# Performance work log

Hardware: AMD Instinct MI355X
Metric: run time of the kernel (lower is better)

Reference implementation:

```python
import jax, jax.numpy as jnp
import numpy as np

N_NODES = 100000
NEG_SLOPE = 0.2
EPS = 1e-16


def gat_conv(x, src, dst, W, a_src, a_dst, bias, heads, out_dim, concat):
    # x: [N, F]; src/dst: [Etot] (self loops already appended)
    N = x.shape[0]
    h = (x @ W).reshape(N, heads, out_dim)          # [N, H, D]
    alpha_src = jnp.einsum('nhd,hd->nh', h, a_src)  # [N, H]
    alpha_dst = jnp.einsum('nhd,hd->nh', h, a_dst)  # [N, H]
    e = alpha_src[src] + alpha_dst[dst]             # [E, H]
    e = jnp.where(e > 0, e, NEG_SLOPE * e)          # leaky_relu
    # segment softmax over incoming edges of each dst node
    m = jax.ops.segment_max(e, dst, num_segments=N)
    e = jnp.exp(e - m[dst])
    s = jax.ops.segment_sum(e, dst, num_segments=N)
    alpha = e / (s[dst] + EPS)                      # [E, H]
    msg = h[src] * alpha[:, :, None]                # [E, H, D]
    out = jax.ops.segment_sum(msg, dst, num_segments=N)  # [N, H, D]
    if concat:
        out = out.reshape(N, heads * out_dim)
    else:
        out = out.mean(axis=1)
    return out + bias


def setup_inputs() -> dict:
    key = jax.random.key(0)
    ks = jax.random.split(key, 10)
    F_in, H1, D1 = 256, 8, 8
    D2 = 256 // 2  # hidden_features // 2
    x = jax.random.normal(ks[0], (N_NODES, F_in), dtype=jnp.float32)
    edge_index = jax.random.randint(ks[1], (2, 1600000), 0, N_NODES, dtype=jnp.int64)
    sc1 = 1.0 / np.sqrt(F_in)
    sc2 = 1.0 / np.sqrt(H1 * D1)
    return {
        'x': x,
        'edge_index': edge_index,
        'W1': jax.random.normal(ks[2], (F_in, H1 * D1), dtype=jnp.float32) * sc1,
        'a_src1': jax.random.normal(ks[3], (H1, D1), dtype=jnp.float32) * 0.1,
        'a_dst1': jax.random.normal(ks[4], (H1, D1), dtype=jnp.float32) * 0.1,
        'b1': jnp.zeros((H1 * D1,), dtype=jnp.float32),
        'W2': jax.random.normal(ks[5], (H1 * D1, D2), dtype=jnp.float32) * sc2,
        'a_src2': jax.random.normal(ks[6], (1, D2), dtype=jnp.float32) * 0.1,
        'a_dst2': jax.random.normal(ks[7], (1, D2), dtype=jnp.float32) * 0.1,
        'b2': jnp.zeros((D2,), dtype=jnp.float32),
    }


def reference(x, edge_index, W1, a_src1, a_dst1, b1, W2, a_src2, a_dst2, b2):
    # GAT.encode in eval mode (dropout p=0.6 disabled)
    N = x.shape[0]
    loop = jnp.arange(N, dtype=edge_index.dtype)
    src = jnp.concatenate([edge_index[0], loop])  # PyG add_self_loops
    dst = jnp.concatenate([edge_index[1], loop])
    h = gat_conv(x, src, dst, W1, a_src1, a_dst1, b1, heads=8, out_dim=8, concat=True)
    h = jax.nn.elu(h)
    z = gat_conv(h, src, dst, W2, a_src2, a_dst2, b2, heads=1, out_dim=128, concat=False)
    return z
```

## Files before the change

### kernel.cpp

```cpp
#include <hip/hip_runtime.h>
#include <hip/hip_bf16.h>
#include <cstdint>

#define H1 8
#define C1 64
#define D2 128
#define FIN 256
#define NEG 0.2f
#define EPSS 1e-16f
#define CH 1024
#define NPW2 8
#define NPB2 32
#define XPAD 264
#define HP 68
#define NPBIN 128
#define TILEB 4096
#define MAXD1 128
#define MAXD2 256

template<typename T> __device__ __forceinline__ float toF(T v);
template<> __device__ __forceinline__ float toF<float>(float v) { return v; }
template<> __device__ __forceinline__ float toF<__hip_bfloat16>(__hip_bfloat16 v) { return __bfloat162float(v); }
template<typename T> __device__ __forceinline__ T fromF(float v);
template<> __device__ __forceinline__ float fromF<float>(float v) { return v; }
template<> __device__ __forceinline__ __hip_bfloat16 fromF<__hip_bfloat16>(float v) { return __float2bfloat16(v); }

__device__ __forceinline__ float bcast_lane(float v, int lane) {
    return __int_as_float(__builtin_amdgcn_readlane(__float_as_int(v), lane));
}

__device__ __forceinline__ unsigned pk_bf16(float lo, float hi) {
    unsigned a = (unsigned)__bfloat16_as_ushort(__float2bfloat16(lo));
    unsigned b = (unsigned)__bfloat16_as_ushort(__float2bfloat16(hi));
    return a | (b << 16);
}

typedef __attribute__((ext_vector_type(8))) short bf16x8;
typedef __attribute__((ext_vector_type(4))) float f32x4;

__device__ __forceinline__ void chain_upd(float ev, float hv,
                                          float& m, float& s, float& a)
{
    float mn = fmaxf(m, ev);
    float sc = __expf(m - mn);
    float p  = __expf(ev - mn);
    s = fmaf(s, sc, p);
    a = fmaf(a, sc, p * hv);
    m = mn;
}

template<typename T>
__global__ __launch_bounds__(256) void k_gemm1(const float* __restrict__ x,
    const float* __restrict__ W1, const float* __restrict__ a_src1,
    const float* __restrict__ a_dst1, T* __restrict__ h1,
    float* __restrict__ asrc1, float* __restrict__ adst1, int N)
{
    __shared__ alignas(16) unsigned short Xs[64 * XPAD];
    __shared__ alignas(16) unsigned short Wt[64 * XPAD];
    int tid = threadIdx.x;
    int wave = tid >> 6, lane = tid & 63;
    int nodeBase = blockIdx.x * 64;

    {
        int c = tid & 63;
        int kb = (tid >> 6) * 4;
        #pragma unroll
        for (int s = 0; s < 16; ++s) {
            int k0 = s * 16 + kb;
            float f0 = W1[(k0 + 0) * C1 + c];
            float f1 = W1[(k0 + 1) * C1 + c];
            float f2 = W1[(k0 + 2) * C1 + c];
            float f3 = W1[(k0 + 3) * C1 + c];
            *reinterpret_cast<uint2*>(&Wt[c * XPAD + k0]) =
                make_uint2(pk_bf16(f0, f1), pk_bf16(f2, f3));
        }
    }
    for (int i = tid; i < 64 * 64; i += 256) {
        int r = i >> 6, kq = i & 63;
        int n = nodeBase + r;
        float4 v = (n < N) ? reinterpret_cast<const float4*>(x)[(size_t)n * 64 + kq]
                           : make_float4(0.f, 0.f, 0.f, 0.f);
        *reinterpret_cast<uint2*>(&Xs[r * XPAD + kq * 4]) =
            make_uint2(pk_bf16(v.x, v.y), pk_bf16(v.z, v.w));
    }
    __syncthreads();

    int m = lane & 15;
    int kg = lane >> 4;
    int arow = wave * 16 + m;
    f32x4 acc[4];
    #pragma unroll
    for (int t = 0; t < 4; ++t) acc[t] = (f32x4){0.f, 0.f, 0.f, 0.f};
    #pragma unroll
    for (int ks = 0; ks < 8; ++ks) {
        int k0 = ks * 32 + kg * 8;
        bf16x8 a = *reinterpret_cast<const bf16x8*>(&Xs[arow * XPAD + k0]);
        #pragma unroll
        for (int t = 0; t < 4; ++t) {
            bf16x8 b = *reinterpret_cast<const bf16x8*>(&Wt[(t * 16 + m) * XPAD + k0]);
            acc[t] = __builtin_amdgcn_mfma_f32_16x16x32_bf16(a, b, acc[t], 0, 0, 0);
        }
    }
    __syncthreads();

    float* Hs = reinterpret_cast<float*>(Xs);
    int crow = (lane >> 4) * 4;
    #pragma unroll
    for (int t = 0; t < 4; ++t)
        #pragma unroll
        for (int r = 0; r < 4; ++r)
            Hs[(wave * 16 + crow + r) * HP + t * 16 + m] = acc[t][r];
    __syncthreads();

    float as_l = a_src1[lane], ad_l = a_dst1[lane];
    int n0 = nodeBase + wave * 16;
    #pragma unroll
    for (int i = 0; i < 16; ++i) {
        int n = n0 + i;
        if (n >= N) break;
        float hv = Hs[(wave * 16 + i) * HP + lane];
        h1[(size_t)n * C1 + lane] = fromF<T>(hv);
        float vs = hv * as_l, vd = hv * ad_l;
        #pragma unroll
        for (int off = 1; off < 8; off <<= 1) {
            vs += __shfl_xor(vs, off);
            vd += __shfl_xor(vd, off);
        }
        if ((lane & 7) == 0) {
            asrc1[n * H1 + (lane >> 3)] = vs;
            adst1[n * H1 + (lane >> 3)] = vd;
        }
    }
}

__global__ __launch_bounds__(128) void k_wvec(const float* __restrict__ W2,
    const float* __restrict__ a_src2, const float* __restrict__ a_dst2,
    float* __restrict__ wsrc, float* __restrict__ wdst)
{
    int t = threadIdx.x;
    int k = t & 63;
    const float* a = (t < 64) ? a_src2 : a_dst2;
    float s = 0.f;
    for (int c = 0; c < D2; ++c) s = fmaf(W2[k * D2 + c], a[c], s);
    if (t < 64) wsrc[k] = s; else wdst[k] = s;
}

__global__ __launch_bounds__(256) void k_binhist(const int* __restrict__ ei, int E, int N,
    int nbins, int* __restrict__ binCnt)
{
    __shared__ int lcnt[1024];
    int tot = E + N;
    int t0 = blockIdx.x * TILEB;
    int cnt = min(TILEB, tot - t0);
    for (int i = threadIdx.x; i < nbins; i += 256) lcnt[i] = 0;
    __syncthreads();
    for (int i = threadIdx.x; i < cnt; i += 256) {
        int e = t0 + i;
        int dst = (e < E) ? ei[(size_t)E + e] : (e - E);
        atomicAdd(&lcnt[dst >> 7], 1);
    }
    __syncthreads();
    for (int i = threadIdx.x; i < nbins; i += 256)
        if (lcnt[i]) atomicAdd(&binCnt[i], lcnt[i]);
}

__global__ __launch_bounds__(256) void k_binscan(const int* __restrict__ binCnt,
    int* __restrict__ binOff, int* __restrict__ binCur, int nbins)
{
    __shared__ int wtot[4];
    int t = threadIdx.x, lane = t & 63, wave = t >> 6;
    int v[4];
    #pragma unroll
    for (int j = 0; j < 4; ++j) {
        int idx = t * 4 + j;
        v[j] = (idx < nbins) ? binCnt[idx] : 0;
    }
    int s = v[0] + v[1] + v[2] + v[3];
    int incl = s;
    #pragma unroll
    for (int off = 1; off < 64; off <<= 1) {
        int tt = __shfl_up(incl, off);
        if (lane >= off) incl += tt;
    }
    if (lane == 63) wtot[wave] = incl;
    __syncthreads();
    int woff = 0;
    #pragma unroll
    for (int w = 0; w < 4; ++w) if (w < wave) woff += wtot[w];
    int run = woff + incl - s;
    #pragma unroll
    for (int j = 0; j < 4; ++j) {
        int idx = t * 4 + j;
        if (idx < nbins) { binOff[idx] = run; binCur[idx] = run; }
        run += v[j];
    }
    if (t == 255) binOff[nbins] = woff + incl;
}

__global__ __launch_bounds__(256) void k_bin(const int* __restrict__ ei, int E, int N,
    int nbins, int* __restrict__ binCur, int* __restrict__ binned)
{
    __shared__ int recs[TILEB];
    __shared__ unsigned short bns[TILEB];
    __shared__ int lcnt[1024];
    __shared__ int lbase[1024];
    int tot = E + N;
    int t0 = blockIdx.x * TILEB;
    int cnt = min(TILEB, tot - t0);
    for (int i = threadIdx.x; i < nbins; i += 256) lcnt[i] = 0;
    __syncthreads();
    for (int i = threadIdx.x; i < cnt; i += 256) {
        int e = t0 + i;
        int src, dst;
        if (e < E) { src = ei[e]; dst = ei[(size_t)E + e]; }
        else       { src = e - E; dst = src; }
        int b = dst >> 7;
        recs[i] = src | ((dst & 127) << 17);
        bns[i] = (unsigned short)b;
        atomicAdd(&lcnt[b], 1);
    }
    __syncthreads();
    for (int i = threadIdx.x; i < nbins; i += 256) {
        int c = lcnt[i];
        if (c) lbase[i] = atomicAdd(&binCur[i], c);
        lcnt[i] = 0;
    }
    __syncthreads();
    for (int i = threadIdx.x; i < cnt; i += 256) {
        int b = bns[i];
        int lp = atomicAdd(&lcnt[b], 1);
        binned[lbase[b] + lp] = recs[i];
    }
}

__global__ __launch_bounds__(256) void k_bindeg(const int* __restrict__ binOff,
    const int* __restrict__ binned, int* __restrict__ deg, int N)
{
    __shared__ int cnt[NPBIN];
    int b = blockIdx.x;
    int s0 = binOff[b], s1 = binOff[b + 1];
    if (threadIdx.x < NPBIN) cnt[threadIdx.x] = 0;
    __syncthreads();
    for (int i = s0 + threadIdx.x; i < s1; i += 256)
        atomicAdd(&cnt[binned[i] >> 17], 1);
    __syncthreads();
    int node = b * NPBIN + threadIdx.x;
    if (threadIdx.x < NPBIN && node < N) deg[node] = cnt[threadIdx.x];
}

__global__ __launch_bounds__(256) void k_binscatter(const int* __restrict__ binOff,
    const int* __restrict__ binned, const int* __restrict__ ptr,
    int* __restrict__ edge_src, int N)
{
    __shared__ int cur[NPBIN];
    int b = blockIdx.x;
    int base = b * NPBIN;
    if (threadIdx.x < NPBIN) {
        int node = base + threadIdx.x;
        cur[threadIdx.x] = (node < N) ? ptr[node] : 0;
    }
    __syncthreads();
    int s0 = binOff[b], s1 = binOff[b + 1];
    for (int i = s0 + threadIdx.x; i < s1; i += 256) {
        int rec = binned[i];
        int p = atomicAdd(&cur[rec >> 17], 1);
        edge_src[p] = rec & 0x1FFFF;
    }
}

__global__ void k_count(const int* __restrict__ ei, int E, int N,
                        int* __restrict__ deg)
{
    int tot = E + N;
    for (int e = blockIdx.x * blockDim.x + threadIdx.x; e < tot;
         e += gridDim.x * blockDim.x) {
        int dst = (e < E) ? ei[(size_t)E + e] : (e - E);
        atomicAdd(&deg[dst], 1);
    }
}

__global__ void k_scatter(const int* __restrict__ ei, int E, int N,
                          int* __restrict__ cursor, int* __restrict__ edge_src)
{
    int tot = E + N;
    for (int e = blockIdx.x * blockDim.x + threadIdx.x; e < tot;
         e += gridDim.x * blockDim.x) {
        int src, dst;
        if (e < E) { src = ei[e]; dst = ei[(size_t)E + e]; }
        else       { src = e - E; dst = e - E; }
        int pos = atomicAdd(&cursor[dst], 1);
        edge_src[pos] = src;
    }
}

__global__ __launch_bounds__(256) void k_scanA(const int* __restrict__ deg,
    int* __restrict__ ptr, int* __restrict__ chunkSum)
{
    __shared__ int wtot[4];
    int b = blockIdx.x, t = threadIdx.x;
    int lane = t & 63, wave = t >> 6;
    int4 v = reinterpret_cast<const int4*>(deg + (size_t)b * CH)[t];
    int s = v.x + v.y + v.z + v.w;
    int incl = s;
    #pragma unroll
    for (int off = 1; off < 64; off <<= 1) {
        int tt = __shfl_up(incl, off);
        if (lane >= off) incl += tt;
    }
    if (lane == 63) wtot[wave] = incl;
    __syncthreads();
    int woff = 0;
    #pragma unroll
    for (int w = 0; w < 4; ++w) if (w < wave) woff += wtot[w];
    int excl = woff + incl - s;
    int i0 = b * CH + t * 4;
    ptr[i0 + 0] = excl;
    ptr[i0 + 1] = excl + v.x;
    ptr[i0 + 2] = excl + v.x + v.y;
    ptr[i0 + 3] = excl + v.x + v.y + v.z;
    if (t == 255) chunkSum[b] = woff + incl;
}

__global__ void k_scanB(const int* __restrict__ chunkSum, int* __restrict__ chunkOff,
                        int NB, int* __restrict__ ptrN)
{
    if (threadIdx.x == 0) {
        int c = 0;
        for (int b = 0; b < NB; ++b) { chunkOff[b] = c; c += chunkSum[b]; }
        *ptrN = c;
    }
}

__global__ __launch_bounds__(256) void k_scanC(int* __restrict__ ptr,
    int* __restrict__ cursor, const int* __restrict__ chunkOff, int N)
{
    int b = blockIdx.x;
    int off = chunkOff[b];
    int i0 = b * CH + threadIdx.x * 4;
    #pragma unroll
    for (int k = 0; k < 4; ++k) {
        int i = i0 + k;
        if (i < N) { int v = ptr[i] + off; ptr[i] = v; cursor[i] = v; }
    }
}

template<typename T>
__global__ __launch_bounds__(256) void k_agg1(const int* __restrict__ ptr,
    const int* __restrict__ edge_src, const T* __restrict__ h1,
    const float* __restrict__ asrc1, const float* __restrict__ adst1,
    const float* __restrict__ b1, const float* __restrict__ wsrc,
    const float* __restrict__ wdst, T* __restrict__ hmid,
    float* __restrict__ asrc2, float* __restrict__ adst2, int N)
{
    __shared__ float S1[4 * MAXD1 * H1];
    int wave = threadIdx.x >> 6, lane = threadIdx.x & 63;
    float* st = S1 + wave * (MAXD1 * H1);
    int n = blockIdx.x * 4 + wave;
    if (n >= N) return;
    int start = ptr[n], end = ptr[n + 1];
    int deg = end - start;
    int h = lane >> 3;
    float o;

    if (deg <= MAXD1) {
        int e_loc = lane >> 3, hh = lane & 7;
        float adsth = adst1[n * H1 + hh];
        float mloc = -1e30f;
        for (int eb = start, base = 0; eb < end; eb += 8, base += 64) {
            int e = eb + e_loc;
            float ev = -1e30f;
            if (e < end) {
                int s = edge_src[e];
                ev = asrc1[s * H1 + hh] + adsth;
                ev = ev > 0.f ? ev : NEG * ev;
                st[base + lane] = ev;
            }
            mloc = fmaxf(mloc, ev);
        }
        mloc = fmaxf(mloc, __shfl_xor(mloc, 8));
        mloc = fmaxf(mloc, __shfl_xor(mloc, 16));
        mloc = fmaxf(mloc, __shfl_xor(mloc, 32));
        __builtin_amdgcn_wave_barrier();
        float sloc = 0.f;
        for (int eb = start, base = 0; eb < end; eb += 8, base += 64) {
            if (eb + e_loc < end) {
                float p = __expf(st[base + lane] - mloc);
                st[base + lane] = p;
                sloc += p;
            }
        }
        sloc += __shfl_xor(sloc, 8);
        sloc += __shfl_xor(sloc, 16);
        sloc += __shfl_xor(sloc, 32);
        float inv = 1.f / (sloc + EPSS);
        __builtin_amdgcn_wave_barrier();
        float inv_c = __shfl(inv, h);

        float a0 = 0.f, a1 = 0.f, a2 = 0.f, a3 = 0.f;
        float a4 = 0.f, a5 = 0.f, a6 = 0.f, a7 = 0.f;
        int e = start;
        for (; e + 8 <= end; e += 8) {
            int r = e - start;
            int i0 = edge_src[e + 0]; int i1 = edge_src[e + 1];
            int i2 = edge_src[e + 2]; int i3 = edge_src[e + 3];
            int i4 = edge_src[e + 4]; int i5 = edge_src[e + 5];
            int i6 = edge_src[e + 6]; int i7 = edge_src[e + 7];
            float w0 = st[(r + 0) * H1 + h]; float w1 = st[(r + 1) * H1 + h];
            float w2 = st[(r + 2) * H1 + h]; float w3 = st[(r + 3) * H1 + h];
            float w4 = st[(r + 4) * H1 + h]; float w5 = st[(r + 5) * H1 + h];
            float w6 = st[(r + 6) * H1 + h]; float w7 = st[(r + 7) * H1 + h];
            a0 = fmaf(w0, toF(h1[((size_t)(unsigned)i0 << 6) + lane]), a0);
            a1 = fmaf(w1, toF(h1[((size_t)(unsigned)i1 << 6) + lane]), a1);
            a2 = fmaf(w2, toF(h1[((size_t)(unsigned)i2 << 6) + lane]), a2);
            a3 = fmaf(w3, toF(h1[((size_t)(unsigned)i3 << 6) + lane]), a3);
            a4 = fmaf(w4, toF(h1[((size_t)(unsigned)i4 << 6) + lane]), a4);
            a5 = fmaf(w5, toF(h1[((size_t)(unsigned)i5 << 6) + lane]), a5);
            a6 = fmaf(w6, toF(h1[((size_t)(unsigned)i6 << 6) + lane]), a6);
            a7 = fmaf(w7, toF(h1[((size_t)(unsigned)i7 << 6) + lane]), a7);
        }
        for (; e < end; ++e) {
            int s = edge_src[e];
            a0 = fmaf(st[(e - start) * H1 + h],
                      toF(h1[((size_t)(unsigned)s << 6) + lane]), a0);
        }
        float acc = ((a0 + a1) + (a2 + a3)) + ((a4 + a5) + (a6 + a7));
        o = acc * inv_c;
    } else {
        float adst = adst1[n * H1 + h];
        float m[8], ss[8], aa[8];
        #pragma unroll
        for (int j = 0; j < 8; ++j) { m[j] = -1e30f; ss[j] = 0.f; aa[j] = 0.f; }
        int e = start;
        for (; e + 8 <= end; e += 8) {
            int idx[8];
            #pragma unroll
            for (int j = 0; j < 8; ++j) idx[j] = edge_src[e + j];
            #pragma unroll
            for (int j = 0; j < 8; ++j) {
                float t = asrc1[idx[j] * H1 + h] + adst;
                t = t > 0.f ? t : NEG * t;
                chain_upd(t, toF(h1[((size_t)(unsigned)idx[j] << 6) + lane]),
                          m[j], ss[j], aa[j]);
            }
        }
        for (; e < end; ++e) {
            int s = edge_src[e];
            float t = asrc1[s * H1 + h] + adst;
            t = t > 0.f ? t : NEG * t;
            chain_upd(t, toF(h1[((size_t)(unsigned)s << 6) + lane]), m[0], ss[0], aa[0]);
        }
        float M = fmaxf(fmaxf(fmaxf(m[0], m[1]), fmaxf(m[2], m[3])),
                        fmaxf(fmaxf(m[4], m[5]), fmaxf(m[6], m[7])));
        float sum = 0.f, acc = 0.f;
        #pragma unroll
        for (int j = 0; j < 8; ++j) {
            float sc = __expf(m[j] - M);
            sum = fmaf(ss[j], sc, sum);
            acc = fmaf(aa[j], sc, acc);
        }
        o = acc / (sum + EPSS);
    }

    o = o + b1[lane];
    o = o > 0.f ? o : (expf(o) - 1.f);
    hmid[(size_t)n * C1 + lane] = fromF<T>(o);
    float vs = o * wsrc[lane];
    float vd = o * wdst[lane];
    #pragma unroll
    for (int off = 1; off < 64; off <<= 1) {
        vs += __shfl_xor(vs, off);
        vd += __shfl_xor(vd, off);
    }
    if (lane == 0) { asrc2[n] = vs; adst2[n] = vd; }
}

template<typename T>
__global__ __launch_bounds__(256) void k_agg2(const int* __restrict__ ptr,
    const int* __restrict__ edge_src, const T* __restrict__ hmid,
    const float* __restrict__ asrc2, const float* __restrict__ adst2,
    T* __restrict__ aggv_out, int N)
{
    __shared__ float S2[4 * MAXD2];
    int wave = threadIdx.x >> 6, lane = threadIdx.x & 63;
    float* st = S2 + wave * MAXD2;
    int n = blockIdx.x * 4 + wave;
    if (n >= N) return;
    int start = ptr[n], end = ptr[n + 1];
    int deg = end - start;
    float adst = adst2[n];
    float aggv;

    if (deg <= MAXD2) {
        float mloc = -1e30f;
        for (int e = start + lane; e < end; e += 64) {
            int s = edge_src[e];
            float ev = asrc2[s] + adst;
            ev = ev > 0.f ? ev : NEG * ev;
            st[e - start] = ev;
            mloc = fmaxf(mloc, ev);
        }
        #pragma unroll
        for (int off = 1; off < 64; off <<= 1)
            mloc = fmaxf(mloc, __shfl_xor(mloc, off));
        __builtin_amdgcn_wave_barrier();
        float sloc = 0.f;
        for (int e = start + lane; e < end; e += 64) {
            float p = __expf(st[e - start] - mloc);
            st[e - start] = p;
            sloc += p;
        }
        #pragma unroll
        for (int off = 1; off < 64; off <<= 1)
            sloc += __shfl_xor(sloc, off);
        float inv = 1.f / (sloc + EPSS);
        __builtin_amdgcn_wave_barrier();

        float a0 = 0.f, a1 = 0.f, a2 = 0.f, a3 = 0.f;
        float a4 = 0.f, a5 = 0.f, a6 = 0.f, a7 = 0.f;
        int e = start;
        for (; e + 8 <= end; e += 8) {
            int r = e - start;
            int i0 = edge_src[e + 0]; int i1 = edge_src[e + 1];
            int i2 = edge_src[e + 2]; int i3 = edge_src[e + 3];
            int i4 = edge_src[e + 4]; int i5 = edge_src[e + 5];
            int i6 = edge_src[e + 6]; int i7 = edge_src[e + 7];
            a0 = fmaf(st[r + 0], toF(hmid[((size_t)(unsigned)i0 << 6) + lane]), a0);
            a1 = fmaf(st[r + 1], toF(hmid[((size_t)(unsigned)i1 << 6) + lane]), a1);
            a2 = fmaf(st[r + 2], toF(hmid[((size_t)(unsigned)i2 << 6) + lane]), a2);
            a3 = fmaf(st[r + 3], toF(hmid[((size_t)(unsigned)i3 << 6) + lane]), a3);
            a4 = fmaf(st[r + 4], toF(hmid[((size_t)(unsigned)i4 << 6) + lane]), a4);
            a5 = fmaf(st[r + 5], toF(hmid[((size_t)(unsigned)i5 << 6) + lane]), a5);
            a6 = fmaf(st[r + 6], toF(hmid[((size_t)(unsigned)i6 << 6) + lane]), a6);
            a7 = fmaf(st[r + 7], toF(hmid[((size_t)(unsigned)i7 << 6) + lane]), a7);
        }
        for (; e < end; ++e) {
            int s = edge_src[e];
            a0 = fmaf(st[e - start], toF(hmid[((size_t)(unsigned)s << 6) + lane]), a0);
        }
        float acc = ((a0 + a1) + (a2 + a3)) + ((a4 + a5) + (a6 + a7));
        aggv = acc * inv;
    } else {
        float m[8], ss[8], aa[8];
        #pragma unroll
        for (int j = 0; j < 8; ++j) { m[j] = -1e30f; ss[j] = 0.f; aa[j] = 0.f; }
        int e = start;
        for (; e + 8 <= end; e += 8) {
            int idx[8];
            #pragma unroll
            for (int j = 0; j < 8; ++j) idx[j] = edge_src[e + j];
            #pragma unroll
            for (int j = 0; j < 8; ++j) {
                float t = asrc2[idx[j]] + adst;
                t = t > 0.f ? t : NEG * t;
                chain_upd(t, toF(hmid[((size_t)(unsigned)idx[j] << 6) + lane]),
                          m[j], ss[j], aa[j]);
            }
        }
        for (; e < end; ++e) {
            int s = edge_src[e];
            float t = asrc2[s] + adst;
            t = t > 0.f ? t : NEG * t;
            chain_upd(t, toF(hmid[((size_t)(unsigned)s << 6) + lane]), m[0], ss[0], aa[0]);
        }
        float M = fmaxf(fmaxf(fmaxf(m[0], m[1]), fmaxf(m[2], m[3])),
                        fmaxf(fmaxf(m[4], m[5]), fmaxf(m[6], m[7])));
        float sum = 0.f, acc = 0.f;
        #pragma unroll
        for (int j = 0; j < 8; ++j) {
            float sc = __expf(m[j] - M);
            sum = fmaf(ss[j], sc, sum);
            acc = fmaf(aa[j], sc, acc);
        }
        aggv = acc / (sum + EPSS);
    }
    aggv_out[(size_t)n * C1 + lane] = fromF<T>(aggv);
}

template<typename T>
__global__ __launch_bounds__(256) void k_gemm2(const T* __restrict__ aggv,
    const float* __restrict__ W2, const float* __restrict__ b2,
    float* __restrict__ out, int N)
{
    __shared__ float Ws[C1 * D2];
    for (int i = threadIdx.x; i < C1 * D2 / 4; i += 256)
        reinterpret_cast<float4*>(Ws)[i] = reinterpret_cast<const float4*>(W2)[i];

    int wave = threadIdx.x >> 6, lane = threadIdx.x & 63;
    int n0 = blockIdx.x * NPB2 + wave * NPW2;

    float av[NPW2];
    #pragma unroll
    for (int j = 0; j < NPW2; ++j) {
        int n = n0 + j;
        av[j] = (n < N) ? toF(aggv[(size_t)n * C1 + lane]) : 0.f;
    }
    __syncthreads();

    float acc0[NPW2], acc1[NPW2];
    #pragma unroll
    for (int j = 0; j < NPW2; ++j) { acc0[j] = 0.f; acc1[j] = 0.f; }

    #pragma unroll 4
    for (int k = 0; k < 64; ++k) {
        float w0 = Ws[k * D2 + lane];
        float w1 = Ws[k * D2 + 64 + lane];
        #pragma unroll
        for (int j = 0; j < NPW2; ++j) {
            float xk = bcast_lane(av[j], k);
            acc0[j] = fmaf(xk, w0, acc0[j]);
            acc1[j] = fmaf(xk, w1, acc1[j]);
        }
    }

    float bb0 = b2[lane], bb1 = b2[64 + lane];
    #pragma unroll
    for (int j = 0; j < NPW2; ++j) {
        int n = n0 + j;
        if (n >= N) continue;
        out[(size_t)n * D2 + lane]      = acc0[j] + bb0;
        out[(size_t)n * D2 + 64 + lane] = acc1[j] + bb1;
    }
}

extern "C" void kernel_launch(void* const* d_in, const int* in_sizes, int n_in,
                              void* d_out, int out_size, void* d_ws, size_t ws_size,
                              hipStream_t stream)
{
    const float* x      = (const float*)d_in[0];
    const int*   ei     = (const int*)d_in[1];
    const float* W1     = (const float*)d_in[2];
    const float* a_src1 = (const float*)d_in[3];
    const float* a_dst1 = (const float*)d_in[4];
    const float* b1     = (const float*)d_in[5];
    const float* W2     = (const float*)d_in[6];
    const float* a_src2 = (const float*)d_in[7];
    const float* a_dst2 = (const float*)d_in[8];
    const float* b2     = (const float*)d_in[9];
    float* out = (float*)d_out;

    const int N = in_sizes[0] / FIN;
    const int E = in_sizes[1] / 2;
    const int Etot = E + N;
    const int NB = (N + CH - 1) / CH;
    const size_t NP = (size_t)NB * CH;

    const size_t common =
        ((size_t)N * H1 * 4 + 255 & ~(size_t)255) * 2 +
        (((size_t)N * 4 + 255) & ~(size_t)255) * 2 +
        512 +
        (((size_t)NP * 4 + 255) & ~(size_t)255) * 2 +
        (((size_t)(NP + 1) * 4 + 255) & ~(size_t)255) +
        (((size_t)NB * 4 + 255) & ~(size_t)255) * 2 +
        (((size_t)Etot * 4 + 255) & ~(size_t)255) +
        4096;
    const bool f32path = ws_size >= common + 2 * ((size_t)N * C1 * 4 + 256);

    char* ws = (char*)d_ws;
    size_t off = 0;
    auto alloc = [&](size_t bytes) -> void* {
        void* p = ws + off;
        off = (off + bytes + 255) & ~(size_t)255;
        return p;
    };
    const size_t es = f32path ? 4 : 2;
    void*  h1v    = alloc((size_t)N * C1 * es);
    void*  hmidv  = alloc((size_t)N * C1 * es);
    float* asrc1  = (float*)alloc((size_t)N * H1 * 4);
    float* adst1  = (float*)alloc((size_t)N * H1 * 4);
    float* asrc2  = (float*)alloc((size_t)N * 4);
    float* adst2  = (float*)alloc((size_t)N * 4);
    float* wsrc   = (float*)alloc(64 * 4);
    float* wdst   = (float*)alloc(64 * 4);
    int*   deg    = (int*)alloc(NP * 4);
    int*   ptr    = (int*)alloc((NP + 1) * 4);
    int*   cursor = (int*)alloc(NP * 4);
    int*   chunkSum = (int*)alloc((size_t)NB * 4);
    int*   chunkOff = (int*)alloc((size_t)NB * 4);
    int*   edge_src = (int*)alloc((size_t)Etot * 4);

    const int nodeBlocks = (N + 3) / 4;
    const int g1Blocks = (N + 63) / 64;
    const int g2Blocks = (N + NPB2 - 1) / NPB2;

    const int nbins = (N + NPBIN - 1) / NPBIN;
    const bool binpath = (N <= (1 << 17)) &&
                         ((size_t)Etot * 4 <= (size_t)N * C1 * es);
    hipMemsetAsync(deg, 0, NP * 4, stream);
    if (binpath) {
        int* binned = (int*)h1v;
        int* binCnt = (int*)hmidv;
        int* binOff = binCnt + 1056;
        int* binCur = binOff + 1056;
        const int binBlocks = (Etot + TILEB - 1) / TILEB;
        hipMemsetAsync(binCnt, 0, (size_t)nbins * 4, stream);
        k_binhist<<<binBlocks, 256, 0, stream>>>(ei, E, N, nbins, binCnt);
        k_binscan<<<1, 256, 0, stream>>>(binCnt, binOff, binCur, nbins);
        k_bin<<<binBlocks, 256, 0, stream>>>(ei, E, N, nbins, binCur, binned);
        k_bindeg<<<nbins, 256, 0, stream>>>(binOff, binned, deg, N);
        k_scanA<<<NB, 256, 0, stream>>>(deg, ptr, chunkSum);
        k_scanB<<<1, 64, 0, stream>>>(chunkSum, chunkOff, NB, ptr + N);
        k_scanC<<<NB, 256, 0, stream>>>(ptr, cursor, chunkOff, N);
        k_binscatter<<<nbins, 256, 0, stream>>>(binOff, binned, ptr, edge_src, N);
    } else {
        k_count<<<2048, 256, 0, stream>>>(ei, E, N, deg);
        k_scanA<<<NB, 256, 0, stream>>>(deg, ptr, chunkSum);
        k_scanB<<<1, 64, 0, stream>>>(chunkSum, chunkOff, NB, ptr + N);
        k_scanC<<<NB, 256, 0, stream>>>(ptr, cursor, chunkOff, N);
        k_scatter<<<2048, 256, 0, stream>>>(ei, E, N, cursor, edge_src);
    }

    k_wvec<<<1, 128, 0, stream>>>(W2, a_src2, a_dst2, wsrc, wdst);

    if (f32path) {
        float* h1 = (float*)h1v; float* hmid = (float*)hmidv;
        k_gemm1<float><<<g1Blocks, 256, 0, stream>>>(x, W1, a_src1, a_dst1, h1, asrc1, adst1, N);
        k_agg1<float><<<nodeBlocks, 256, 0, stream>>>(ptr, edge_src, h1, asrc1, adst1, b1,
                                                      wsrc, wdst, hmid, asrc2, adst2, N);
        float* aggv = (float*)h1v;
        k_agg2<float><<<nodeBlocks, 256, 0, stream>>>(ptr, edge_src, hmid, asrc2, adst2, aggv, N);
        k_gemm2<float><<<g2Blocks, 256, 0, stream>>>(aggv, W2, b2, out, N);
    } else {
        __hip_bfloat16* h1 = (__hip_bfloat16*)h1v; __hip_bfloat16* hmid = (__hip_bfloat16*)hmidv;
        k_gemm1<__hip_bfloat16><<<g1Blocks, 256, 0, stream>>>(x, W1, a_src1, a_dst1, h1, asrc1, adst1, N);
        k_agg1<__hip_bfloat16><<<nodeBlocks, 256, 0, stream>>>(ptr, edge_src, h1, asrc1, adst1, b1,
                                                               wsrc, wdst, hmid, asrc2, adst2, N);
        __hip_bfloat16* aggv = (__hip_bfloat16*)h1v;
        k_agg2<__hip_bfloat16><<<nodeBlocks, 256, 0, stream>>>(ptr, edge_src, hmid, asrc2, adst2, aggv, N);
        k_gemm2<__hip_bfloat16><<<g2Blocks, 256, 0, stream>>>(aggv, W2, b2, out, N);
    }
}
```

Baseline: 371.2 us.

## Fuse bin degree count, CSR scan and scatter into one kernel; deepen gather unroll

The binned CSR build now runs as a single kernel per bin. It counts per-node degrees in shared memory, does a local wave prefix scan offset by the bin's global start, writes ptr and scatters edge sources. This replaces the degree kernel, the three-kernel global scan and the separate scatter kernel, along with the memset of deg, which cuts launches and global round trips. Separately, the aggregation loops in both layers gain a 16-edge unrolled stage that issues all gathers before the FMAs to raise memory-level parallelism, at some cost in register pressure.

Result: faster. 358.9 us (-3.3%).

```diff
diff --git a/kernel.cpp b/kernel.cpp
--- a/kernel.cpp
+++ b/kernel.cpp
@@ -233,35 +233,43 @@
     }
 }
 
-__global__ __launch_bounds__(256) void k_bindeg(const int* __restrict__ binOff,
-    const int* __restrict__ binned, int* __restrict__ deg, int N)
+__global__ __launch_bounds__(256) void k_binptr(const int* __restrict__ binOff,
+    const int* __restrict__ binned, int* __restrict__ ptr,
+    int* __restrict__ edge_src, int N, int nbins)
 {
     __shared__ int cnt[NPBIN];
-    int b = blockIdx.x;
+    __shared__ int cur[NPBIN];
+    __shared__ int w0tot;
+    int b = blockIdx.x, t = threadIdx.x;
     int s0 = binOff[b], s1 = binOff[b + 1];
-    if (threadIdx.x < NPBIN) cnt[threadIdx.x] = 0;
-    __syncthreads();
-    for (int i = s0 + threadIdx.x; i < s1; i += 256)
+    if (t < NPBIN) cnt[t] = 0;
+    __syncthreads();
+    for (int i = s0 + t; i < s1; i += 256)
         atomicAdd(&cnt[binned[i] >> 17], 1);
     __syncthreads();
-    int node = b * NPBIN + threadIdx.x;
-    if (threadIdx.x < NPBIN && node < N) deg[node] = cnt[threadIdx.x];
-}
-
-__global__ __launch_bounds__(256) void k_binscatter(const int* __restrict__ binOff,
-    const int* __restrict__ binned, const int* __restrict__ ptr,
-    int* __restrict__ edge_src, int N)
-{
-    __shared__ int cur[NPBIN];
-    int b = blockIdx.x;
-    int base = b * NPBIN;
-    if (threadIdx.x < NPBIN) {
-        int node = base + threadIdx.x;
-        cur[threadIdx.x] = (node < N) ? ptr[node] : 0;
-    }
-    __syncthreads();
-    int s0 = binOff[b], s1 = binOff[b + 1];
-    for (int i = s0 + threadIdx.x; i < s1; i += 256) {
+    int v = 0, incl = 0;
+    if (t < NPBIN) {
+        int lane = t & 63;
+        v = cnt[t];
+        incl = v;
+        #pragma unroll
+        for (int off = 1; off < 64; off <<= 1) {
+            int tt = __shfl_up(incl, off);
+            if (lane >= off) incl += tt;
+        }
+        if (t == 63) w0tot = incl;
+    }
+    __syncthreads();
+    if (t < NPBIN) {
+        int base = s0 + ((t >= 64) ? w0tot : 0);
+        int excl = base + incl - v;
+        int node = b * NPBIN + t;
+        if (node < N) ptr[node] = excl;
+        cur[t] = excl;
+    }
+    if (b == nbins - 1 && t == 0) ptr[N] = s1;
+    __syncthreads();
+    for (int i = s0 + t; i < s1; i += 256) {
         int rec = binned[i];
         int p = atomicAdd(&cur[rec >> 17], 1);
         edge_src[p] = rec & 0x1FFFF;
@@ -399,24 +407,44 @@
         float a0 = 0.f, a1 = 0.f, a2 = 0.f, a3 = 0.f;
         float a4 = 0.f, a5 = 0.f, a6 = 0.f, a7 = 0.f;
         int e = start;
+        for (; e + 16 <= end; e += 16) {
+            int r = e - start;
+            int idx[16];
+            #pragma unroll
+            for (int j = 0; j < 16; ++j) idx[j] = edge_src[e + j];
+            float hv[16];
+            #pragma unroll
+            for (int j = 0; j < 16; ++j)
+                hv[j] = toF(h1[((size_t)(unsigned)idx[j] << 6) + lane]);
+            float w[16];
+            #pragma unroll
+            for (int j = 0; j < 16; ++j) w[j] = st[(r + j) * H1 + h];
+            a0 = fmaf(w[0],  hv[0],  a0); a1 = fmaf(w[1],  hv[1],  a1);
+            a2 = fmaf(w[2],  hv[2],  a2); a3 = fmaf(w[3],  hv[3],  a3);
+            a4 = fmaf(w[4],  hv[4],  a4); a5 = fmaf(w[5],  hv[5],  a5);
+            a6 = fmaf(w[6],  hv[6],  a6); a7 = fmaf(w[7],  hv[7],  a7);
+            a0 = fmaf(w[8],  hv[8],  a0); a1 = fmaf(w[9],  hv[9],  a1);
+            a2 = fmaf(w[10], hv[10], a2); a3 = fmaf(w[11], hv[11], a3);
+            a4 = fmaf(w[12], hv[12], a4); a5 = fmaf(w[13], hv[13], a5);
+            a6 = fmaf(w[14], hv[14], a6); a7 = fmaf(w[15], hv[15], a7);
+        }
         for (; e + 8 <= end; e += 8) {
             int r = e - start;
-            int i0 = edge_src[e + 0]; int i1 = edge_src[e + 1];
-            int i2 = edge_src[e + 2]; int i3 = edge_src[e + 3];
-            int i4 = edge_src[e + 4]; int i5 = edge_src[e + 5];
-            int i6 = edge_src[e + 6]; int i7 = edge_src[e + 7];
-            float w0 = st[(r + 0) * H1 + h]; float w1 = st[(r + 1) * H1 + h];
-            float w2 = st[(r + 2) * H1 + h]; float w3 = st[(r + 3) * H1 + h];
-            float w4 = st[(r + 4) * H1 + h]; float w5 = st[(r + 5) * H1 + h];
-            float w6 = st[(r + 6) * H1 + h]; float w7 = st[(r + 7) * H1 + h];
-            a0 = fmaf(w0, toF(h1[((size_t)(unsigned)i0 << 6) + lane]), a0);
-            a1 = fmaf(w1, toF(h1[((size_t)(unsigned)i1 << 6) + lane]), a1);
-            a2 = fmaf(w2, toF(h1[((size_t)(unsigned)i2 << 6) + lane]), a2);
-            a3 = fmaf(w3, toF(h1[((size_t)(unsigned)i3 << 6) + lane]), a3);
-            a4 = fmaf(w4, toF(h1[((size_t)(unsigned)i4 << 6) + lane]), a4);
-            a5 = fmaf(w5, toF(h1[((size_t)(unsigned)i5 << 6) + lane]), a5);
-            a6 = fmaf(w6, toF(h1[((size_t)(unsigned)i6 << 6) + lane]), a6);
-            a7 = fmaf(w7, toF(h1[((size_t)(unsigned)i7 << 6) + lane]), a7);
+            int idx[8];
+            #pragma unroll
+            for (int j = 0; j < 8; ++j) idx[j] = edge_src[e + j];
+            float hv[8];
+            #pragma unroll
+            for (int j = 0; j < 8; ++j)
+                hv[j] = toF(h1[((size_t)(unsigned)idx[j] << 6) + lane]);
+            a0 = fmaf(st[(r + 0) * H1 + h], hv[0], a0);
+            a1 = fmaf(st[(r + 1) * H1 + h], hv[1], a1);
+            a2 = fmaf(st[(r + 2) * H1 + h], hv[2], a2);
+            a3 = fmaf(st[(r + 3) * H1 + h], hv[3], a3);
+            a4 = fmaf(st[(r + 4) * H1 + h], hv[4], a4);
+            a5 = fmaf(st[(r + 5) * H1 + h], hv[5], a5);
+            a6 = fmaf(st[(r + 6) * H1 + h], hv[6], a6);
+            a7 = fmaf(st[(r + 7) * H1 + h], hv[7], a7);
         }
         for (; e < end; ++e) {
             int s = edge_src[e];
@@ -518,20 +546,37 @@
         float a0 = 0.f, a1 = 0.f, a2 = 0.f, a3 = 0.f;
         float a4 = 0.f, a5 = 0.f, a6 = 0.f, a7 = 0.f;
         int e = start;
+        for (; e + 16 <= end; e += 16) {
+            int r = e - start;
+            int idx[16];
+            #pragma unroll
+            for (int j = 0; j < 16; ++j) idx[j] = edge_src[e + j];
+            float hv[16];
+            #pragma unroll
+            for (int j = 0; j < 16; ++j)
+                hv[j] = toF(hmid[((size_t)(unsigned)idx[j] << 6) + lane]);
+            a0 = fmaf(st[r + 0],  hv[0],  a0); a1 = fmaf(st[r + 1],  hv[1],  a1);
+            a2 = fmaf(st[r + 2],  hv[2],  a2); a3 = fmaf(st[r + 3],  hv[3],  a3);
+            a4 = fmaf(st[r + 4],  hv[4],  a4); a5 = fmaf(st[r + 5],  hv[5],  a5);
+            a6 = fmaf(st[r + 6],  hv[6],  a6); a7 = fmaf(st[r + 7],  hv[7],  a7);
+            a0 = fmaf(st[r + 8],  hv[8],  a0); a1 = fmaf(st[r + 9],  hv[9],  a1);
+            a2 = fmaf(st[r + 10], hv[10], a2); a3 = fmaf(st[r + 11], hv[11], a3);
+            a4 = fmaf(st[r + 12], hv[12], a4); a5 = fmaf(st[r + 13], hv[13], a5);
+            a6 = fmaf(st[r + 14], hv[14], a6); a7 = fmaf(st[r + 15], hv[15], a7);
+        }
         for (; e + 8 <= end; e += 8) {
             int r = e - start;
-            int i0 = edge_src[e + 0]; int i1 = edge_src[e + 1];
-            int i2 = edge_src[e + 2]; int i3 = edge_src[e + 3];
-            int i4 = edge_src[e + 4]; int i5 = edge_src[e + 5];
-            int i6 = edge_src[e + 6]; int i7 = edge_src[e + 7];
-            a0 = fmaf(st[r + 0], toF(hmid[((size_t)(unsigned)i0 << 6) + lane]), a0);
-            a1 = fmaf(st[r + 1], toF(hmid[((size_t)(unsigned)i1 << 6) + lane]), a1);
-            a2 = fmaf(st[r + 2], toF(hmid[((size_t)(unsigned)i2 << 6) + lane]), a2);
-            a3 = fmaf(st[r + 3], toF(hmid[((size_t)(unsigned)i3 << 6) + lane]), a3);
-            a4 = fmaf(st[r + 4], toF(hmid[((size_t)(unsigned)i4 << 6) + lane]), a4);
-            a5 = fmaf(st[r + 5], toF(hmid[((size_t)(unsigned)i5 << 6) + lane]), a5);
-            a6 = fmaf(st[r + 6], toF(hmid[((size_t)(unsigned)i6 << 6) + lane]), a6);
-            a7 = fmaf(st[r + 7], toF(hmid[((size_t)(unsigned)i7 << 6) + lane]), a7);
+            int idx[8];
+            #pragma unroll
+            for (int j = 0; j < 8; ++j) idx[j] = edge_src[e + j];
+            float hv[8];
+            #pragma unroll
+            for (int j = 0; j < 8; ++j)
+                hv[j] = toF(hmid[((size_t)(unsigned)idx[j] << 6) + lane]);
+            a0 = fmaf(st[r + 0], hv[0], a0); a1 = fmaf(st[r + 1], hv[1], a1);
+            a2 = fmaf(st[r + 2], hv[2], a2); a3 = fmaf(st[r + 3], hv[3], a3);
+            a4 = fmaf(st[r + 4], hv[4], a4); a5 = fmaf(st[r + 5], hv[5], a5);
+            a6 = fmaf(st[r + 6], hv[6], a6); a7 = fmaf(st[r + 7], hv[7], a7);
         }
         for (; e < end; ++e) {
             int s = edge_src[e];
@@ -685,7 +730,6 @@
     const int nbins = (N + NPBIN - 1) / NPBIN;
     const bool binpath = (N <= (1 << 17)) &&
                          ((size_t)Etot * 4 <= (size_t)N * C1 * es);
-    hipMemsetAsync(deg, 0, NP * 4, stream);
     if (binpath) {
         int* binned = (int*)h1v;
         int* binCnt = (int*)hmidv;
@@ -696,12 +740,9 @@
         k_binhist<<<binBlocks, 256, 0, stream>>>(ei, E, N, nbins, binCnt);
         k_binscan<<<1, 256, 0, stream>>>(binCnt, binOff, binCur, nbins);
         k_bin<<<binBlocks, 256, 0, stream>>>(ei, E, N, nbins, binCur, binned);
-        k_bindeg<<<nbins, 256, 0, stream>>>(binOff, binned, deg, N);
-        k_scanA<<<NB, 256, 0, stream>>>(deg, ptr, chunkSum);
-        k_scanB<<<1, 64, 0, stream>>>(chunkSum, chunkOff, NB, ptr + N);
-        k_scanC<<<NB, 256, 0, stream>>>(ptr, cursor, chunkOff, N);
-        k_binscatter<<<nbins, 256, 0, stream>>>(binOff, binned, ptr, edge_src, N);
+        k_binptr<<<nbins, 256, 0, stream>>>(binOff, binned, ptr, edge_src, N, nbins);
     } else {
+        hipMemsetAsync(deg, 0, NP * 4, stream);
         k_count<<<2048, 256, 0, stream>>>(ei, E, N, deg);
         k_scanA<<<NB, 256, 0, stream>>>(deg, ptr, chunkSum);
         k_scanB<<<1, 64, 0, stream>>>(chunkSum, chunkOff, NB, ptr + N);
```

## Fuse bin degree, scan and scatter into one kernel; precompute bf16 W1

Applied to the files above, without the earlier changes.

In the bin path, one kernel per bin now counts degrees, does the prefix sum, writes ptr and scatters edges. This is possible because bins are already contiguous in global order. It replaces the bindeg, three scan kernels, binscatter and the deg memset, removing several launches and round trips through global memory. Separately, W1 is converted to padded bf16 once by a new small kernel. gemm1 then splits K into two halves, which shrinks its shared memory so more blocks can be resident, at the cost of an extra barrier per half.

New measurement: 344.6 us. 1.08x faster.

```diff
diff --git a/kernel.cpp b/kernel.cpp
--- a/kernel.cpp
+++ b/kernel.cpp
@@ -12,6 +12,7 @@
 #define NPW2 8
 #define NPB2 32
 #define XPAD 264
+#define XH 136
 #define HP 68
 #define NPBIN 128
 #define TILEB 4096
@@ -49,59 +50,64 @@
     m = mn;
 }
 
+__global__ __launch_bounds__(256) void k_wcvt(const float* __restrict__ W1,
+    unsigned short* __restrict__ Wb)
+{
+    int t = blockIdx.x * 256 + threadIdx.x;
+    int c = t >> 7, kp = t & 127;
+    if (c < C1) {
+        float f0 = W1[(2 * kp) * C1 + c];
+        float f1 = W1[(2 * kp + 1) * C1 + c];
+        *reinterpret_cast<unsigned*>(&Wb[c * XPAD + 2 * kp]) = pk_bf16(f0, f1);
+    }
+}
+
 template<typename T>
 __global__ __launch_bounds__(256) void k_gemm1(const float* __restrict__ x,
-    const float* __restrict__ W1, const float* __restrict__ a_src1,
+    const unsigned short* __restrict__ Wb, const float* __restrict__ a_src1,
     const float* __restrict__ a_dst1, T* __restrict__ h1,
     float* __restrict__ asrc1, float* __restrict__ adst1, int N)
 {
-    __shared__ alignas(16) unsigned short Xs[64 * XPAD];
-    __shared__ alignas(16) unsigned short Wt[64 * XPAD];
+    __shared__ alignas(16) unsigned short Xs[64 * XH];
+    __shared__ alignas(16) unsigned short Wt[64 * XH];
     int tid = threadIdx.x;
     int wave = tid >> 6, lane = tid & 63;
     int nodeBase = blockIdx.x * 64;
-
-    {
-        int c = tid & 63;
-        int kb = (tid >> 6) * 4;
-        #pragma unroll
-        for (int s = 0; s < 16; ++s) {
-            int k0 = s * 16 + kb;
-            float f0 = W1[(k0 + 0) * C1 + c];
-            float f1 = W1[(k0 + 1) * C1 + c];
-            float f2 = W1[(k0 + 2) * C1 + c];
-            float f3 = W1[(k0 + 3) * C1 + c];
-            *reinterpret_cast<uint2*>(&Wt[c * XPAD + k0]) =
-                make_uint2(pk_bf16(f0, f1), pk_bf16(f2, f3));
-        }
-    }
-    for (int i = tid; i < 64 * 64; i += 256) {
-        int r = i >> 6, kq = i & 63;
-        int n = nodeBase + r;
-        float4 v = (n < N) ? reinterpret_cast<const float4*>(x)[(size_t)n * 64 + kq]
-                           : make_float4(0.f, 0.f, 0.f, 0.f);
-        *reinterpret_cast<uint2*>(&Xs[r * XPAD + kq * 4]) =
-            make_uint2(pk_bf16(v.x, v.y), pk_bf16(v.z, v.w));
-    }
-    __syncthreads();
-
-    int m = lane & 15;
-    int kg = lane >> 4;
+    int m = lane & 15, kg = lane >> 4;
     int arow = wave * 16 + m;
+
     f32x4 acc[4];
     #pragma unroll
     for (int t = 0; t < 4; ++t) acc[t] = (f32x4){0.f, 0.f, 0.f, 0.f};
-    #pragma unroll
-    for (int ks = 0; ks < 8; ++ks) {
-        int k0 = ks * 32 + kg * 8;
-        bf16x8 a = *reinterpret_cast<const bf16x8*>(&Xs[arow * XPAD + k0]);
-        #pragma unroll
-        for (int t = 0; t < 4; ++t) {
-            bf16x8 b = *reinterpret_cast<const bf16x8*>(&Wt[(t * 16 + m) * XPAD + k0]);
-            acc[t] = __builtin_amdgcn_mfma_f32_16x16x32_bf16(a, b, acc[t], 0, 0, 0);
-        }
-    }
-    __syncthreads();
+
+    #pragma unroll
+    for (int kh = 0; kh < 2; ++kh) {
+        for (int i = tid; i < 1024; i += 256) {
+            int c = i >> 4, ch = i & 15;
+            *reinterpret_cast<uint4*>(&Wt[c * XH + ch * 8]) =
+                *reinterpret_cast<const uint4*>(&Wb[c * XPAD + kh * 128 + ch * 8]);
+        }
+        for (int i = tid; i < 2048; i += 256) {
+            int r = i >> 5, q = i & 31;
+            int n = nodeBase + r;
+            float4 v = (n < N) ? reinterpret_cast<const float4*>(x)[(size_t)n * 64 + kh * 32 + q]
+                               : make_float4(0.f, 0.f, 0.f, 0.f);
+            *reinterpret_cast<uint2*>(&Xs[r * XH + q * 4]) =
+                make_uint2(pk_bf16(v.x, v.y), pk_bf16(v.z, v.w));
+        }
+        __syncthreads();
+        #pragma unroll
+        for (int ks = 0; ks < 4; ++ks) {
+            int k0 = ks * 32 + kg * 8;
+            bf16x8 a = *reinterpret_cast<const bf16x8*>(&Xs[arow * XH + k0]);
+            #pragma unroll
+            for (int t = 0; t < 4; ++t) {
+                bf16x8 b = *reinterpret_cast<const bf16x8*>(&Wt[(t * 16 + m) * XH + k0]);
+                acc[t] = __builtin_amdgcn_mfma_f32_16x16x32_bf16(a, b, acc[t], 0, 0, 0);
+            }
+        }
+        __syncthreads();
+    }
 
     float* Hs = reinterpret_cast<float*>(Xs);
     int crow = (lane >> 4) * 4;
@@ -233,35 +239,43 @@
     }
 }
 
-__global__ __launch_bounds__(256) void k_bindeg(const int* __restrict__ binOff,
-    const int* __restrict__ binned, int* __restrict__ deg, int N)
+__global__ __launch_bounds__(256) void k_binptr(const int* __restrict__ binOff,
+    const int* __restrict__ binned, int* __restrict__ ptr,
+    int* __restrict__ edge_src, int N, int nbins)
 {
     __shared__ int cnt[NPBIN];
-    int b = blockIdx.x;
+    __shared__ int cur[NPBIN];
+    __shared__ int w0tot;
+    int b = blockIdx.x, t = threadIdx.x;
     int s0 = binOff[b], s1 = binOff[b + 1];
-    if (threadIdx.x < NPBIN) cnt[threadIdx.x] = 0;
-    __syncthreads();
-    for (int i = s0 + threadIdx.x; i < s1; i += 256)
+    if (t < NPBIN) cnt[t] = 0;
+    __syncthreads();
+    for (int i = s0 + t; i < s1; i += 256)
         atomicAdd(&cnt[binned[i] >> 17], 1);
     __syncthreads();
-    int node = b * NPBIN + threadIdx.x;
-    if (threadIdx.x < NPBIN && node < N) deg[node] = cnt[threadIdx.x];
-}
-
-__global__ __launch_bounds__(256) void k_binscatter(const int* __restrict__ binOff,
-    const int* __restrict__ binned, const int* __restrict__ ptr,
-    int* __restrict__ edge_src, int N)
-{
-    __shared__ int cur[NPBIN];
-    int b = blockIdx.x;
-    int base = b * NPBIN;
-    if (threadIdx.x < NPBIN) {
-        int node = base + threadIdx.x;
-        cur[threadIdx.x] = (node < N) ? ptr[node] : 0;
-    }
-    __syncthreads();
-    int s0 = binOff[b], s1 = binOff[b + 1];
-    for (int i = s0 + threadIdx.x; i < s1; i += 256) {
+    int v = 0, incl = 0;
+    if (t < NPBIN) {
+        int lane = t & 63;
+        v = cnt[t];
+        incl = v;
+        #pragma unroll
+        for (int off = 1; off < 64; off <<= 1) {
+            int tt = __shfl_up(incl, off);
+            if (lane >= off) incl += tt;
+        }
+        if (t == 63) w0tot = incl;
+    }
+    __syncthreads();
+    if (t < NPBIN) {
+        int base = s0 + ((t >= 64) ? w0tot : 0);
+        int excl = base + incl - v;
+        int node = b * NPBIN + t;
+        if (node < N) ptr[node] = excl;
+        cur[t] = excl;
+    }
+    if (b == nbins - 1 && t == 0) ptr[N] = s1;
+    __syncthreads();
+    for (int i = s0 + t; i < s1; i += 256) {
         int rec = binned[i];
         int p = atomicAdd(&cur[rec >> 17], 1);
         edge_src[p] = rec & 0x1FFFF;
@@ -652,6 +666,7 @@
         (((size_t)(NP + 1) * 4 + 255) & ~(size_t)255) +
         (((size_t)NB * 4 + 255) & ~(size_t)255) * 2 +
         (((size_t)Etot * 4 + 255) & ~(size_t)255) +
+        (64 * XPAD * 2 + 256) +
         4096;
     const bool f32path = ws_size >= common + 2 * ((size_t)N * C1 * 4 + 256);
 
@@ -677,15 +692,17 @@
     int*   chunkSum = (int*)alloc((size_t)NB * 4);
     int*   chunkOff = (int*)alloc((size_t)NB * 4);
     int*   edge_src = (int*)alloc((size_t)Etot * 4);
+    unsigned short* Wb = (unsigned short*)alloc(64 * XPAD * 2);
 
     const int nodeBlocks = (N + 3) / 4;
     const int g1Blocks = (N + 63) / 64;
     const int g2Blocks = (N + NPB2 - 1) / NPB2;
 
+    k_wcvt<<<32, 256, 0, stream>>>(W1, Wb);
+
     const int nbins = (N + NPBIN - 1) / NPBIN;
     const bool binpath = (N <= (1 << 17)) &&
                          ((size_t)Etot * 4 <= (size_t)N * C1 * es);
-    hipMemsetAsync(deg, 0, NP * 4, stream);
     if (binpath) {
         int* binned = (int*)h1v;
         int* binCnt = (int*)hmidv;
@@ -696,12 +713,9 @@
         k_binhist<<<binBlocks, 256, 0, stream>>>(ei, E, N, nbins, binCnt);
         k_binscan<<<1, 256, 0, stream>>>(binCnt, binOff, binCur, nbins);
         k_bin<<<binBlocks, 256, 0, stream>>>(ei, E, N, nbins, binCur, binned);
-        k_bindeg<<<nbins, 256, 0, stream>>>(binOff, binned, deg, N);
-        k_scanA<<<NB, 256, 0, stream>>>(deg, ptr, chunkSum);
-        k_scanB<<<1, 64, 0, stream>>>(chunkSum, chunkOff, NB, ptr + N);
-        k_scanC<<<NB, 256, 0, stream>>>(ptr, cursor, chunkOff, N);
-        k_binscatter<<<nbins, 256, 0, stream>>>(binOff, binned, ptr, edge_src, N);
+        k_binptr<<<nbins, 256, 0, stream>>>(binOff, binned, ptr, edge_src, N, nbins);
     } else {
+        hipMemsetAsync(deg, 0, NP * 4, stream);
         k_count<<<2048, 256, 0, stream>>>(ei, E, N, deg);
         k_scanA<<<NB, 256, 0, stream>>>(deg, ptr, chunkSum);
         k_scanB<<<1, 64, 0, stream>>>(chunkSum, chunkOff, NB, ptr + N);
@@ -713,7 +727,7 @@
 
     if (f32path) {
         float* h1 = (float*)h1v; float* hmid = (float*)hmidv;
-        k_gemm1<float><<<g1Blocks, 256, 0, stream>>>(x, W1, a_src1, a_dst1, h1, asrc1, adst1, N);
+        k_gemm1<float><<<g1Blocks, 256, 0, stream>>>(x, Wb, a_src1, a_dst1, h1, asrc1, adst1, N);
         k_agg1<float><<<nodeBlocks, 256, 0, stream>>>(ptr, edge_src, h1, asrc1, adst1, b1,
                                                       wsrc, wdst, hmid, asrc2, adst2, N);
         float* aggv = (float*)h1v;
@@ -721,7 +735,7 @@
         k_gemm2<float><<<g2Blocks, 256, 0, stream>>>(aggv, W2, b2, out, N);
     } else {
         __hip_bfloat16* h1 = (__hip_bfloat16*)h1v; __hip_bfloat16* hmid = (__hip_bfloat16*)hmidv;
-        k_gemm1<__hip_bfloat16><<<g1Blocks, 256, 0, stream>>>(x, W1, a_src1, a_dst1, h1, asrc1, adst1, N);
+        k_gemm1<__hip_bfloat16><<<g1Blocks, 256, 0, stream>>>(x, Wb, a_src1, a_dst1, h1, asrc1, adst1, N);
         k_agg1<__hip_bfloat16><<<nodeBlocks, 256, 0, stream>>>(ptr, edge_src, h1, asrc1, adst1, b1,
                                                                wsrc, wdst, hmid, asrc2, adst2, N);
         __hip_bfloat16* aggv = (__hip_bfloat16*)h1v;
```
